# Performance work log

Measured on AMD Instinct MI355X. Metric: run time of the kernel, lower is better.

## Reference

```python
import jax, jax.numpy as jnp
import numpy as np

C_IN, C_OUT = 128, 128
B, H, W = 16, 192, 192


def _conv(x, w, pad):
    # x: NCHW, w: OIHW, pad: ((ph,ph),(pw,pw))
    return jax.lax.conv_general_dilated(
        x, w, window_strides=(1, 1), padding=pad,
        dimension_numbers=('NCHW', 'OIHW', 'NCHW'))


def _diag_masks(dtype=jnp.float32):
    eye = jnp.eye(3, dtype=dtype)            # mask_19: mask[c, c] = 1
    anti = eye[::-1, :]                      # mask_37: mask[2-c, c] = 1
    return eye[None, None], anti[None, None] # broadcast to (O,I,3,3)


def setup_inputs() -> dict:
    key = jax.random.key(0)
    ks = jax.random.split(key, 6)
    return {
        'x': jax.random.normal(ks[0], (B, C_IN, H, W), dtype=jnp.float32),
        'w_square': jax.random.normal(ks[1], (C_OUT, C_IN, 3, 3), dtype=jnp.float32) * 0.05,
        'w_ver': jax.random.normal(ks[2], (C_OUT, C_IN, 3, 1), dtype=jnp.float32) * 0.05,
        'w_hor': jax.random.normal(ks[3], (C_OUT, C_IN, 1, 3), dtype=jnp.float32) * 0.05,
        'w_diag19': jax.random.normal(ks[4], (C_OUT, C_IN, 3, 3), dtype=jnp.float32) * 0.05,
        'w_diag37': jax.random.normal(ks[5], (C_OUT, C_IN, 3, 3), dtype=jnp.float32) * 0.05,
    }


def reference(x, w_square, w_ver, w_hor, w_diag19, w_diag37):
    m19, m37 = _diag_masks(x.dtype)
    out = _conv(x, w_square, ((1, 1), (1, 1)))
    out = out + _conv(x, w_ver, ((1, 1), (0, 0)))
    out = out + _conv(x, w_hor, ((0, 0), (1, 1)))
    out = out + _conv(x, w_diag19 * m19, ((1, 1), (1, 1)))
    out = out + _conv(x, w_diag37 * m37, ((1, 1), (1, 1)))
    return out
```

## Files before the change

kernel.cpp:

```cpp
#include <hip/hip_runtime.h>

#define HH 192
#define WW 192
#define HWPIX (HH * WW)

typedef __attribute__((ext_vector_type(8))) short bf16x8;
typedef __attribute__((ext_vector_type(4))) float f32x4;
typedef __attribute__((ext_vector_type(4))) unsigned int u32x4;

__device__ __forceinline__ unsigned f2bf(float f) {
    unsigned u = __builtin_bit_cast(unsigned, f);
    return (u + 0x7FFFu + ((u >> 16) & 1u)) >> 16;
}

__device__ __forceinline__ unsigned cvtpk(float lo, float hi) {
    unsigned r;
    asm("v_cvt_pk_bf16_f32 %0, %1, %2" : "=v"(r) : "v"(lo), "v"(hi));
    return r;
}

__global__ void fuse_weights(const float* __restrict__ wsq, const float* __restrict__ wv,
                             const float* __restrict__ whr, const float* __restrict__ w19,
                             const float* __restrict__ w37, unsigned short* __restrict__ wbuf) {
    int idx = blockIdx.x * 256 + threadIdx.x;
    if (idx >= 128 * 128 * 9) return;
    int o = idx / 1152;
    int r = idx - o * 1152;
    int c = r / 9;
    int tap = r - c * 9;
    int kh = tap / 3, kw = tap - kh * 3;
    float v = wsq[((o * 128 + c) * 3 + kh) * 3 + kw];
    if (kw == 1) v += wv[(o * 128 + c) * 3 + kh];
    if (kh == 1) v += whr[(o * 128 + c) * 3 + kw];
    if (kh == kw) v += w19[((o * 128 + c) * 3 + kh) * 3 + kw];
    if (kh + kw == 2) v += w37[((o * 128 + c) * 3 + kh) * 3 + kw];
    int cc = c >> 5, ow = o >> 4;
    int ln = ((c >> 3) & 3) * 16 + (o & 15);
    int j = c & 7;
    int frag = ((cc * 3 + kw) * 3 + kh) * 8 + ow;
    wbuf[(size_t)frag * 512 + ln * 8 + j] = (unsigned short)f2bf(v);
}

__global__ __launch_bounds__(256, 2) void convg(const float* __restrict__ x,
                                                const unsigned short* __restrict__ wbuf,
                                                float* __restrict__ out) {
    const int t = threadIdx.x, l = t & 63, ni = t >> 6;
    const int l15 = l & 15, l4 = l >> 4;

    int id = (int)blockIdx.x;
    int id2 = (id & 7) * 288 + (id >> 3);
    int b = id2 / 144;
    int rem = id2 - b * 144;
    int by = rem / 12, bx = rem - by * 12;
    const int h0 = by * 16, w0 = bx * 16;

    const float* __restrict__ xb = x + (size_t)b * (128 * HWPIX);

    f32x4 acc[8][4];
    const f32x4 zero = {0.f, 0.f, 0.f, 0.f};
#pragma unroll
    for (int ow = 0; ow < 8; ++ow)
#pragma unroll
        for (int np = 0; np < 4; ++np) acc[ow][np] = zero;

    int ghc[6], hok[6];
#pragma unroll
    for (int rid = 0; rid < 6; ++rid) {
        int gh = h0 + 4 * ni - 1 + rid;
        hok[rid] = (unsigned)gh < (unsigned)HH;
        ghc[rid] = min(max(gh, 0), HH - 1);
    }

    float fv[6][8];
    bf16x8 Bc[6];

#define LOADI(IT)                                                                        \
    {                                                                                    \
        int cc_ = (IT) / 3, kw_ = (IT) - 3 * cc_;                                        \
        int gw = w0 - 1 + kw_ + l15;                                                     \
        int gwc = min(max(gw, 0), WW - 1);                                               \
        const float* pb = xb + (size_t)(cc_ * 32 + l4 * 8) * HWPIX + gwc;                \
        _Pragma("unroll") for (int rid = 0; rid < 6; ++rid) {                            \
            const float* p = pb + ghc[rid] * WW;                                         \
            _Pragma("unroll") for (int j = 0; j < 8; ++j)                                \
                fv[rid][j] = p[(size_t)j * HWPIX];                                       \
        }                                                                                \
    }

#define PACKI(IT)                                                                        \
    {                                                                                    \
        int cc_ = (IT) / 3, kw_ = (IT) - 3 * cc_;                                        \
        (void)cc_;                                                                       \
        int gw = w0 - 1 + kw_ + l15;                                                     \
        int wok = (unsigned)gw < (unsigned)WW;                                           \
        _Pragma("unroll") for (int rid = 0; rid < 6; ++rid) {                            \
            int ok = wok & hok[rid];                                                     \
            u32x4 pk;                                                                    \
            _Pragma("unroll") for (int q = 0; q < 4; ++q) {                              \
                unsigned v = cvtpk(fv[rid][2 * q], fv[rid][2 * q + 1]);                  \
                pk[q] = ok ? v : 0u;                                                     \
            }                                                                            \
            Bc[rid] = __builtin_bit_cast(bf16x8, pk);                                    \
        }                                                                                \
    }

#define MMI(IT)                                                                          \
    {                                                                                    \
        int cc_ = (IT) / 3, kw_ = (IT) - 3 * cc_;                                        \
        const unsigned short* wp =                                                       \
            wbuf + (size_t)((cc_ * 3 + kw_) * 3) * 8 * 512 + l * 8;                      \
        _Pragma("unroll") for (int ow = 0; ow < 8; ++ow) {                               \
            bf16x8 a0 = *(const bf16x8*)(wp + (0 * 8 + ow) * 512);                       \
            bf16x8 a1 = *(const bf16x8*)(wp + (1 * 8 + ow) * 512);                       \
            bf16x8 a2 = *(const bf16x8*)(wp + (2 * 8 + ow) * 512);                       \
            _Pragma("unroll") for (int np = 0; np < 4; ++np)                             \
                acc[ow][np] = __builtin_amdgcn_mfma_f32_16x16x32_bf16(                   \
                    a0, Bc[np + 0], acc[ow][np], 0, 0, 0);                               \
            _Pragma("unroll") for (int np = 0; np < 4; ++np)                             \
                acc[ow][np] = __builtin_amdgcn_mfma_f32_16x16x32_bf16(                   \
                    a1, Bc[np + 1], acc[ow][np], 0, 0, 0);                               \
            _Pragma("unroll") for (int np = 0; np < 4; ++np)                             \
                acc[ow][np] = __builtin_amdgcn_mfma_f32_16x16x32_bf16(                   \
                    a2, Bc[np + 2], acc[ow][np], 0, 0, 0);                               \
        }                                                                                \
    }

    LOADI(0)
#pragma unroll 1
    for (int it = 0; it < 12; ++it) {
        PACKI(it)
        int itn = it < 11 ? it + 1 : 11;
        LOADI(itn)
        MMI(it)
    }

    float* __restrict__ ob =
        out + (size_t)b * (128 * HWPIX) + (size_t)(h0 + 4 * ni) * WW + w0 + l15;
#pragma unroll
    for (int ow = 0; ow < 8; ++ow) {
#pragma unroll
        for (int j = 0; j < 4; ++j) {
            int o = ow * 16 + l4 * 4 + j;
            float* op = ob + (size_t)o * HWPIX;
#pragma unroll
            for (int np = 0; np < 4; ++np)
                op[np * WW] = acc[ow][np][j];
        }
    }
}

extern "C" void kernel_launch(void* const* d_in, const int* in_sizes, int n_in,
                              void* d_out, int out_size, void* d_ws, size_t ws_size,
                              hipStream_t stream) {
    const float* x   = (const float*)d_in[0];
    const float* wsq = (const float*)d_in[1];
    const float* wvv = (const float*)d_in[2];
    const float* wh  = (const float*)d_in[3];
    const float* w19 = (const float*)d_in[4];
    const float* w37 = (const float*)d_in[5];

    unsigned short* wbuf = (unsigned short*)d_ws;

    fuse_weights<<<576, 256, 0, stream>>>(wsq, wvv, wh, w19, w37, wbuf);
    convg<<<2304, 256, 0, stream>>>(x, wbuf, (float*)d_out);
}
```

Baseline: 316.2 us.

## Replace cross-iteration input prefetch with in-iteration double-buffered rows for occupancy

```diff
diff --git a/kernel.cpp b/kernel.cpp
--- a/kernel.cpp
+++ b/kernel.cpp
@@ -41,7 +41,7 @@
     wbuf[(size_t)frag * 512 + ln * 8 + j] = (unsigned short)f2bf(v);
 }
 
-__global__ __launch_bounds__(256, 2) void convg(const float* __restrict__ x,
+__global__ __launch_bounds__(256, 3) void convg(const float* __restrict__ x,
                                                 const unsigned short* __restrict__ wbuf,
                                                 float* __restrict__ out) {
     const int t = threadIdx.x, l = t & 63, ni = t >> 6;
@@ -71,37 +71,31 @@
         ghc[rid] = min(max(gh, 0), HH - 1);
     }
 
-    float fv[6][8];
+    float fvA[8], fvB[8];
     bf16x8 Bc[6];
 
-#define LOADI(IT)                                                                        \
+#define LOADROW(IT, RID, SV)                                                             \
     {                                                                                    \
         int cc_ = (IT) / 3, kw_ = (IT) - 3 * cc_;                                        \
         int gw = w0 - 1 + kw_ + l15;                                                     \
         int gwc = min(max(gw, 0), WW - 1);                                               \
-        const float* pb = xb + (size_t)(cc_ * 32 + l4 * 8) * HWPIX + gwc;                \
-        _Pragma("unroll") for (int rid = 0; rid < 6; ++rid) {                            \
-            const float* p = pb + ghc[rid] * WW;                                         \
-            _Pragma("unroll") for (int j = 0; j < 8; ++j)                                \
-                fv[rid][j] = p[(size_t)j * HWPIX];                                       \
-        }                                                                                \
+        const float* p_ =                                                                \
+            xb + (size_t)(cc_ * 32 + l4 * 8) * HWPIX + ghc[RID] * WW + gwc;              \
+        _Pragma("unroll") for (int j = 0; j < 8; ++j) SV[j] = p_[(size_t)j * HWPIX];     \
     }
 
-#define PACKI(IT)                                                                        \
+#define PACKROW(IT, RID, SV)                                                             \
     {                                                                                    \
         int cc_ = (IT) / 3, kw_ = (IT) - 3 * cc_;                                        \
         (void)cc_;                                                                       \
         int gw = w0 - 1 + kw_ + l15;                                                     \
-        int wok = (unsigned)gw < (unsigned)WW;                                           \
-        _Pragma("unroll") for (int rid = 0; rid < 6; ++rid) {                            \
-            int ok = wok & hok[rid];                                                     \
-            u32x4 pk;                                                                    \
-            _Pragma("unroll") for (int q = 0; q < 4; ++q) {                              \
-                unsigned v = cvtpk(fv[rid][2 * q], fv[rid][2 * q + 1]);                  \
-                pk[q] = ok ? v : 0u;                                                     \
-            }                                                                            \
-            Bc[rid] = __builtin_bit_cast(bf16x8, pk);                                    \
+        int ok = ((unsigned)gw < (unsigned)WW) & hok[RID];                               \
+        u32x4 pk;                                                                        \
+        _Pragma("unroll") for (int q = 0; q < 4; ++q) {                                  \
+            unsigned v_ = cvtpk(SV[2 * q], SV[2 * q + 1]);                               \
+            pk[q] = ok ? v_ : 0u;                                                        \
         }                                                                                \
+        Bc[RID] = __builtin_bit_cast(bf16x8, pk);                                        \
     }
 
 #define MMI(IT)                                                                          \
@@ -125,12 +119,20 @@
         }                                                                                \
     }
 
-    LOADI(0)
 #pragma unroll 1
     for (int it = 0; it < 12; ++it) {
-        PACKI(it)
-        int itn = it < 11 ? it + 1 : 11;
-        LOADI(itn)
+        LOADROW(it, 0, fvA)
+        LOADROW(it, 1, fvB)
+        PACKROW(it, 0, fvA)
+        LOADROW(it, 2, fvA)
+        PACKROW(it, 1, fvB)
+        LOADROW(it, 3, fvB)
+        PACKROW(it, 2, fvA)
+        LOADROW(it, 4, fvA)
+        PACKROW(it, 3, fvB)
+        LOADROW(it, 5, fvB)
+        PACKROW(it, 4, fvA)
+        PACKROW(it, 5, fvB)
         MMI(it)
     }
 
```

New measurement: 1.072 ms (median of 2 runs). 239% more time.
